# Kernel optimization log

Hardware: AMD Instinct MI355X
Metric: run time of the kernel (lower is better)

The kernel has to match this reference:

```python
import jax, jax.numpy as jnp
import numpy as np

N = 100000   # nodes
E = 1600000  # edges (avg degree 16)
D = 128      # feature dim (in_size == out_size)
L = 3        # n_layers

def setup_inputs() -> dict:
    key = jax.random.key(0)
    k0, k1, k2, k3, k4 = jax.random.split(key, 5)
    x = jax.random.normal(k0, (N, D), dtype=jnp.float32)
    src = jax.random.randint(k1, (E,), 0, N)
    dst = jax.random.randint(k2, (E,), 0, N)
    # positive edge weights (DGL EdgeWeightNorm requires nonnegative)
    edge_weight = jax.random.uniform(k3, (E,), dtype=jnp.float32) + 0.1
    W = jax.random.normal(k4, (L, D, D), dtype=jnp.float32) / np.float32(np.sqrt(D))
    b = jnp.zeros((L, D), dtype=jnp.float32)
    return {"x": x, "edge_weight": edge_weight, "W": W, "b": b, "src": src, "dst": dst}

def reference(x, edge_weight, W, b, src, dst):
    n = x.shape[0]
    # EdgeWeightNorm(norm='both'): w_ij / sqrt(deg_out_w(src_i) * deg_in_w(dst_j))
    deg_src = jax.ops.segment_sum(edge_weight, src, num_segments=n)  # weighted out-degree
    deg_dst = jax.ops.segment_sum(edge_weight, dst, num_segments=n)  # weighted in-degree
    nw = edge_weight * jax.lax.rsqrt(deg_src[src] * deg_dst[dst])    # [E]
    h = x
    for i in range(W.shape[0]):
        # GraphConv(norm='none'): transform, weighted-sum aggregate, bias, ELU
        h = h @ W[i]                                   # [N, D]
        msg = h[src] * nw[:, None]                     # [E, D] gather + scale
        h = jax.ops.segment_sum(msg, dst, num_segments=n) + b[i]
        h = jax.nn.elu(h)
    return h
```

## Files before the change

### kernel.cpp

```cpp
#include <hip/hip_runtime.h>
#include <hip/hip_bf16.h>


#define D128 128
#define PBLK 256
#define BUCKET_SHIFT 8
#define DCAP 7168

typedef __attribute__((ext_vector_type(8))) short s8v;
typedef __attribute__((ext_vector_type(16))) float f16v;

__device__ __forceinline__ float elu1(float x) {
    return x > 0.f ? x : (expf(x) - 1.f);
}

__device__ __forceinline__ unsigned short bf16_rne(float v) {
    unsigned u = __float_as_uint(v);
    return (unsigned short)((u + 0x7fffu + ((u >> 16) & 1u)) >> 16);
}


__global__ __launch_bounds__(256) void part_hist2(
    const int* __restrict__ src, const int* __restrict__ dst,
    int* __restrict__ histT2, int E, int nb, int chunk, int hlen) {
    extern __shared__ int sh[];
    for (int i = threadIdx.x; i < 2 * nb; i += 256) sh[i] = 0;
    __syncthreads();
    int b = blockIdx.x;
    int beg = b * chunk, end = min(E, beg + chunk);
    for (int e = beg + threadIdx.x; e < end; e += 256) {
        atomicAdd(&sh[dst[e] >> BUCKET_SHIFT], 1);
        atomicAdd(&sh[nb + (src[e] >> BUCKET_SHIFT)], 1);
    }
    __syncthreads();
    for (int i = threadIdx.x; i < nb; i += 256)
        histT2[i * PBLK + b] = sh[i];
    for (int i = threadIdx.x; i < nb; i += 256)
        histT2[hlen + i * PBLK + b] = sh[nb + i];
}

__global__ __launch_bounds__(256) void scan_block(
    int* __restrict__ data, int* __restrict__ blockSums, int n) {
    __shared__ int tmp[256];
    int gid = blockIdx.x * 256 + threadIdx.x;
    int v = (gid < n) ? data[gid] : 0;
    tmp[threadIdx.x] = v;
    __syncthreads();
    for (int off = 1; off < 256; off <<= 1) {
        int t = (threadIdx.x >= off) ? tmp[threadIdx.x - off] : 0;
        __syncthreads();
        tmp[threadIdx.x] += t;
        __syncthreads();
    }
    if (gid < n) data[gid] = tmp[threadIdx.x] - v;
    if (threadIdx.x == 255) blockSums[blockIdx.x] = tmp[255];
}

__global__ __launch_bounds__(1024) void scan_sums(int* __restrict__ bsums, int nb) {
    __shared__ int tmp[1024];
    int v = (threadIdx.x < nb) ? bsums[threadIdx.x] : 0;
    tmp[threadIdx.x] = v;
    __syncthreads();
    for (int off = 1; off < 1024; off <<= 1) {
        int t = (threadIdx.x >= off) ? tmp[threadIdx.x - off] : 0;
        __syncthreads();
        tmp[threadIdx.x] += t;
        __syncthreads();
    }
    if (threadIdx.x < nb) bsums[threadIdx.x] = tmp[threadIdx.x] - v;
}

__global__ __launch_bounds__(256) void part_scatter2(
    const int* __restrict__ src, const int* __restrict__ dst,
    const float* __restrict__ w, const int* __restrict__ offsT2,
    const int* __restrict__ bsums,
    int2* __restrict__ pkw, int2* __restrict__ skw,
    int E, int nb, int chunk, int hlen) {
    extern __shared__ int cur[];
    int b = blockIdx.x;
    for (int i = threadIdx.x; i < nb; i += 256)
        cur[i] = offsT2[i * PBLK + b] + bsums[i];
    for (int i = threadIdx.x; i < nb; i += 256)
        cur[nb + i] = offsT2[hlen + i * PBLK + b] + bsums[nb + i] - E;
    __syncthreads();
    int beg = b * chunk, end = min(E, beg + chunk);
    for (int e = beg + threadIdx.x; e < end; e += 256) {
        int d = dst[e];
        int s = src[e];
        int wv = __float_as_int(w[e]);
        int kd = d >> BUCKET_SHIFT;
        int pos = atomicAdd(&cur[kd], 1);
        pkw[pos] = make_int2((int)((unsigned)s | ((unsigned)(d & 255) << 24)), wv);
        int ks = s >> BUCKET_SHIFT;
        int posS = atomicAdd(&cur[nb + ks], 1);
        skw[posS] = make_int2(s & 255, wv);
    }
}

__global__ __launch_bounds__(256) void bucket_sumS(
    const int2* __restrict__ skw, const int* __restrict__ offsT2,
    const int* __restrict__ bsums,
    float* __restrict__ deg_src, int E, int nb, int N, int hlen) {
    __shared__ float wsum[256];
    int k = blockIdx.x;
    int base = offsT2[hlen + k * PBLK] + bsums[nb + k] - E;
    int end = (k + 1 < nb) ? (offsT2[hlen + (k + 1) * PBLK] + bsums[nb + k + 1] - E) : E;
    int t = threadIdx.x;
    wsum[t] = 0.f;
    __syncthreads();
    for (int i = base + t; i < end; i += 256) {
        int2 v = skw[i];
        atomicAdd(&wsum[v.x], __int_as_float(v.y));
    }
    __syncthreads();
    int node = (k << BUCKET_SHIFT) + t;
    if (node < N) deg_src[node] = wsum[t];
}

__global__ __launch_bounds__(256) void bucket_build(
    const int2* __restrict__ pkw, const int* __restrict__ offsT,
    const int* __restrict__ bsums, const float* __restrict__ deg_src,
    int* __restrict__ row_start, int2* __restrict__ edata,
    int E, int nb, int N) {
    __shared__ int cnt[256];
    __shared__ float wsum[256];
    __shared__ int loc[256];
    __shared__ int cur2[256];
    extern __shared__ int2 stage[];

    int k = blockIdx.x;
    int base = offsT[k * PBLK] + bsums[k];
    int end = (k + 1 < nb) ? (offsT[(k + 1) * PBLK] + bsums[k + 1]) : E;
    int m = end - base;
    int t = threadIdx.x;
    cnt[t] = 0;
    wsum[t] = 0.f;
    __syncthreads();
    bool staged = (m <= DCAP);
    for (int i = t; i < m; i += 256) {
        int2 kw = pkw[base + i];
        if (staged) stage[i] = kw;
        int dl = (unsigned)kw.x >> 24;
        atomicAdd(&cnt[dl], 1);
        atomicAdd(&wsum[dl], __int_as_float(kw.y));
    }
    __syncthreads();
    int v = cnt[t];
    loc[t] = v;
    __syncthreads();
    for (int off = 1; off < 256; off <<= 1) {
        int tv = (t >= off) ? loc[t - off] : 0;
        __syncthreads();
        loc[t] += tv;
        __syncthreads();
    }
    int excl = loc[t] - v;
    loc[t] = excl;
    cur2[t] = 0;
    int node = (k << BUCKET_SHIFT) + t;
    if (node < N) row_start[node] = base + excl;
    if (k == 0 && t == 0) row_start[N] = E;
    __syncthreads();
    for (int i = t; i < m; i += 256) {
        int2 kw = staged ? stage[i] : pkw[base + i];
        int dl = (unsigned)kw.x >> 24;
        int s = kw.x & 0xFFFFFF;
        int pos = base + loc[dl] + atomicAdd(&cur2[dl], 1);
        float nw = __int_as_float(kw.y) * rsqrtf(deg_src[s] * wsum[dl]);
        edata[pos] = make_int2(s, __float_as_int(nw));
    }
}


__global__ __launch_bounds__(256) void prep_w(
    const float* __restrict__ W, unsigned short* __restrict__ Wh,
    unsigned short* __restrict__ Wl, int total) {
    int i = blockIdx.x * 256 + threadIdx.x;
    if (i >= total) return;
    int l = i >> 14;
    int rem = i & 16383;
    int k = rem >> 7, nn = rem & 127;
    float v = W[i];
    unsigned short h = bf16_rne(v);
    float fh = __uint_as_float((unsigned)h << 16);
    unsigned short lo = bf16_rne(v - fh);
    size_t oi = ((((size_t)l * 16 + (k >> 3)) * 128 + nn) << 3) + (k & 7);
    Wh[oi] = h;
    Wl[oi] = lo;
}

__global__ __launch_bounds__(256) void gemm_mfma_f32(
    const float* __restrict__ A, const unsigned short* __restrict__ Wh,
    const unsigned short* __restrict__ Wl, unsigned short* __restrict__ Hb,
    int n) {
    __shared__ s8v lds_hi[16][32];
    __shared__ s8v lds_lo[16][32];
    const int t = threadIdx.x;
    const int r0 = blockIdx.x * 32;
    const int l = t & 63;
    const int wv = t >> 6;
    const int n0 = wv * 32;
    const int lr = l & 31, lh = l >> 5;

    s8v bh[8], bl[8];
#pragma unroll
    for (int k0 = 0; k0 < 8; ++k0) {
        int kc = k0 * 2 + lh;
        size_t gi = ((size_t)kc * 128 + n0 + lr) << 3;
        bh[k0] = *(const s8v*)(Wh + gi);
        bl[k0] = *(const s8v*)(Wl + gi);
    }

    {
        int row = t >> 3;
        int kc0 = t & 7;
        int r = r0 + row;
#pragma unroll
        for (int hhalf = 0; hhalf < 2; ++hhalf) {
            int kc = kc0 + 8 * hhalf;
            float4 v0 = make_float4(0.f, 0.f, 0.f, 0.f), v1 = v0;
            if (r < n) {
                const float4* ap = (const float4*)(A + (size_t)r * D128 + kc * 8);
                v0 = ap[0];
                v1 = ap[1];
            }
            s8v sh, sl;
#pragma unroll
            for (int e = 0; e < 8; ++e) {
                float v = (e < 4) ? ((const float*)&v0)[e] : ((const float*)&v1)[e - 4];
                unsigned short h = bf16_rne(v);
                float fh = __uint_as_float((unsigned)h << 16);
                sh[e] = (short)h;
                sl[e] = (short)bf16_rne(v - fh);
            }
            lds_hi[kc][row ^ (kc & 7)] = sh;
            lds_lo[kc][row ^ (kc & 7)] = sl;
        }
    }
    __syncthreads();

    f16v acc = {0.f, 0.f, 0.f, 0.f, 0.f, 0.f, 0.f, 0.f,
                0.f, 0.f, 0.f, 0.f, 0.f, 0.f, 0.f, 0.f};
#pragma unroll
    for (int k0 = 0; k0 < 8; ++k0) {
        int kc = k0 * 2 + lh;
        s8v ah = lds_hi[kc][lr ^ (kc & 7)];
        s8v al = lds_lo[kc][lr ^ (kc & 7)];
        acc = __builtin_amdgcn_mfma_f32_32x32x16_bf16(ah, bh[k0], acc, 0, 0, 0);
        acc = __builtin_amdgcn_mfma_f32_32x32x16_bf16(ah, bl[k0], acc, 0, 0, 0);
        acc = __builtin_amdgcn_mfma_f32_32x32x16_bf16(al, bh[k0], acc, 0, 0, 0);
    }

#pragma unroll
    for (int rg = 0; rg < 16; ++rg) {
        int grow = r0 + (rg & 3) + 8 * (rg >> 2) + 4 * lh;
        if (grow < n) Hb[(size_t)grow * D128 + n0 + lr] = bf16_rne(acc[rg]);
    }
}

__global__ __launch_bounds__(256) void gemm_mfma_bf16(
    const unsigned short* __restrict__ A, const unsigned short* __restrict__ Wh,
    const unsigned short* __restrict__ Wl, unsigned short* __restrict__ Hb,
    int n) {
    __shared__ s8v lds_a[16][64];
    const int t = threadIdx.x;
    const int r0 = blockIdx.x * 64;
    const int l = t & 63;
    const int wv = t >> 6;
    const int n0 = wv * 32;
    const int lr = l & 31, lh = l >> 5;

    s8v bh[8], bl[8];
#pragma unroll
    for (int k0 = 0; k0 < 8; ++k0) {
        int kc = k0 * 2 + lh;
        size_t gi = ((size_t)kc * 128 + n0 + lr) << 3;
        bh[k0] = *(const s8v*)(Wh + gi);
        bl[k0] = *(const s8v*)(Wl + gi);
    }

#pragma unroll
    for (int g4 = 0; g4 < 4; ++g4) {
        int g = t * 4 + g4;
        int row = g >> 4, kc = g & 15;
        int r = r0 + row;
        s8v v = {0, 0, 0, 0, 0, 0, 0, 0};
        if (r < n) v = *(const s8v*)(A + (size_t)r * D128 + kc * 8);
        lds_a[kc][row ^ (kc & 7)] = v;
    }
    __syncthreads();

    f16v acc0 = {0.f, 0.f, 0.f, 0.f, 0.f, 0.f, 0.f, 0.f,
                 0.f, 0.f, 0.f, 0.f, 0.f, 0.f, 0.f, 0.f};
    f16v acc1 = acc0;
#pragma unroll
    for (int k0 = 0; k0 < 8; ++k0) {
        int kc = k0 * 2 + lh;
        s8v a0 = lds_a[kc][lr ^ (kc & 7)];
        s8v a1 = lds_a[kc][(32 + lr) ^ (kc & 7)];
        acc0 = __builtin_amdgcn_mfma_f32_32x32x16_bf16(a0, bh[k0], acc0, 0, 0, 0);
        acc0 = __builtin_amdgcn_mfma_f32_32x32x16_bf16(a0, bl[k0], acc0, 0, 0, 0);
        acc1 = __builtin_amdgcn_mfma_f32_32x32x16_bf16(a1, bh[k0], acc1, 0, 0, 0);
        acc1 = __builtin_amdgcn_mfma_f32_32x32x16_bf16(a1, bl[k0], acc1, 0, 0, 0);
    }

#pragma unroll
    for (int rg = 0; rg < 16; ++rg) {
        int rr = (rg & 3) + 8 * (rg >> 2) + 4 * lh;
        int grow0 = r0 + rr;
        int grow1 = r0 + 32 + rr;
        if (grow0 < n) Hb[(size_t)grow0 * D128 + n0 + lr] = bf16_rne(acc0[rg]);
        if (grow1 < n) Hb[(size_t)grow1 * D128 + n0 + lr] = bf16_rne(acc1[rg]);
    }
}


__global__ __launch_bounds__(256) void aggregate_bf16(
    const unsigned short* __restrict__ hb, const int* __restrict__ rs,
    const int2* __restrict__ edata, const float* __restrict__ bias,
    unsigned short* __restrict__ outb, float* __restrict__ outf,
    int obf, int n) {
    int wave = threadIdx.x >> 6;
    int lane = threadIdx.x & 63;
    int node = blockIdx.x * 4 + wave;
    if (node >= n) return;
    int beg = rs[node], end = rs[node + 1];
    int half = lane >> 5, c = lane & 31;
    float4 a0 = make_float4(0.f, 0.f, 0.f, 0.f);
    float4 a1 = a0, a2 = a0, a3 = a0;
    int i = beg + half;
    for (; i + 6 < end; i += 8) {
        int2 e0 = edata[i];
        int2 e1 = edata[i + 2];
        int2 e2 = edata[i + 4];
        int2 e3 = edata[i + 6];
        uint2 p0 = ((const uint2*)(hb + (size_t)e0.x * D128))[c];
        uint2 p1 = ((const uint2*)(hb + (size_t)e1.x * D128))[c];
        uint2 p2 = ((const uint2*)(hb + (size_t)e2.x * D128))[c];
        uint2 p3 = ((const uint2*)(hb + (size_t)e3.x * D128))[c];
        float w0 = __int_as_float(e0.y), w1 = __int_as_float(e1.y);
        float w2 = __int_as_float(e2.y), w3 = __int_as_float(e3.y);
        a0.x = fmaf(__uint_as_float(p0.x << 16), w0, a0.x);
        a0.y = fmaf(__uint_as_float(p0.x & 0xffff0000u), w0, a0.y);
        a0.z = fmaf(__uint_as_float(p0.y << 16), w0, a0.z);
        a0.w = fmaf(__uint_as_float(p0.y & 0xffff0000u), w0, a0.w);
        a1.x = fmaf(__uint_as_float(p1.x << 16), w1, a1.x);
        a1.y = fmaf(__uint_as_float(p1.x & 0xffff0000u), w1, a1.y);
        a1.z = fmaf(__uint_as_float(p1.y << 16), w1, a1.z);
        a1.w = fmaf(__uint_as_float(p1.y & 0xffff0000u), w1, a1.w);
        a2.x = fmaf(__uint_as_float(p2.x << 16), w2, a2.x);
        a2.y = fmaf(__uint_as_float(p2.x & 0xffff0000u), w2, a2.y);
        a2.z = fmaf(__uint_as_float(p2.y << 16), w2, a2.z);
        a2.w = fmaf(__uint_as_float(p2.y & 0xffff0000u), w2, a2.w);
        a3.x = fmaf(__uint_as_float(p3.x << 16), w3, a3.x);
        a3.y = fmaf(__uint_as_float(p3.x & 0xffff0000u), w3, a3.y);
        a3.z = fmaf(__uint_as_float(p3.y << 16), w3, a3.z);
        a3.w = fmaf(__uint_as_float(p3.y & 0xffff0000u), w3, a3.w);
    }
    for (; i < end; i += 2) {
        int2 e0 = edata[i];
        uint2 p0 = ((const uint2*)(hb + (size_t)e0.x * D128))[c];
        float w0 = __int_as_float(e0.y);
        a0.x = fmaf(__uint_as_float(p0.x << 16), w0, a0.x);
        a0.y = fmaf(__uint_as_float(p0.x & 0xffff0000u), w0, a0.y);
        a0.z = fmaf(__uint_as_float(p0.y << 16), w0, a0.z);
        a0.w = fmaf(__uint_as_float(p0.y & 0xffff0000u), w0, a0.w);
    }
    a0.x += a1.x + a2.x + a3.x;
    a0.y += a1.y + a2.y + a3.y;
    a0.z += a1.z + a2.z + a3.z;
    a0.w += a1.w + a2.w + a3.w;
    a0.x += __shfl_xor(a0.x, 32);
    a0.y += __shfl_xor(a0.y, 32);
    a0.z += __shfl_xor(a0.z, 32);
    a0.w += __shfl_xor(a0.w, 32);
    if (half == 0) {
        float4 bb = ((const float4*)bias)[c];
        float4 o;
        o.x = elu1(a0.x + bb.x);
        o.y = elu1(a0.y + bb.y);
        o.z = elu1(a0.z + bb.z);
        o.w = elu1(a0.w + bb.w);
        if (obf) {
            uint2 p;
            p.x = (unsigned)bf16_rne(o.x) | ((unsigned)bf16_rne(o.y) << 16);
            p.y = (unsigned)bf16_rne(o.z) | ((unsigned)bf16_rne(o.w) << 16);
            ((uint2*)(outb + (size_t)node * D128))[c] = p;
        } else {
            ((float4*)(outf + (size_t)node * D128))[c] = o;
        }
    }
}

extern "C" void kernel_launch(void* const* d_in, const int* in_sizes, int n_in,
                              void* d_out, int out_size, void* d_ws, size_t ws_size,
                              hipStream_t stream) {
    const float* x   = (const float*)d_in[0];
    const float* ew  = (const float*)d_in[1];
    const float* W   = (const float*)d_in[2];
    const float* b   = (const float*)d_in[3];
    const int*   src = (const int*)d_in[4];
    const int*   dst = (const int*)d_in[5];
    float* out = (float*)d_out;

    const int N = in_sizes[0] / D128;
    const int E = in_sizes[1];
    const int L = in_sizes[2] / (D128 * D128);
    const int nb = (N + 255) >> BUCKET_SHIFT;
    const int hlen = nb * PBLK;

    char* ws = (char*)d_ws;
    size_t off = 0;
    auto take = [&](size_t bytes) {
        void* p = ws + off;
        off = (off + bytes + 255) & ~(size_t)255;
        return p;
    };
    float* deg_src = (float*)take((size_t)N * 4);
    int*   histT2  = (int*)take((size_t)2 * hlen * 4);
    int*   bsums   = (int*)take(1024 * 4);
    int*   rstart  = (int*)take((size_t)(N + 1) * 4);
    int2*  edata   = (int2*)take((size_t)E * 8);
    unsigned short* Hb = (unsigned short*)take((size_t)N * D128 * 2);
    unsigned short* Ab = (unsigned short*)take((size_t)N * D128 * 2);
    unsigned short* Whg = (unsigned short*)take((size_t)L * D128 * D128 * 2);
    unsigned short* Wlg = (unsigned short*)take((size_t)L * D128 * D128 * 2);
    int2* pkw = (int2*)Ab;
    int2* skw = ((int2*)Ab) + E;

    const int chunk = (E + PBLK - 1) / PBLK;
    const int sb2 = (2 * hlen + 255) / 256;
    const size_t part_lds = (size_t)2 * nb * 4;
    const size_t dcap_lds = (size_t)DCAP * 8;

    const int wtotal = L * D128 * D128;
    prep_w<<<(wtotal + 255) / 256, 256, 0, stream>>>(W, Whg, Wlg, wtotal);

    part_hist2<<<PBLK, 256, part_lds, stream>>>(src, dst, histT2, E, nb, chunk, hlen);
    scan_block<<<sb2, 256, 0, stream>>>(histT2, bsums, 2 * hlen);
    scan_sums<<<1, 1024, 0, stream>>>(bsums, sb2);
    part_scatter2<<<PBLK, 256, part_lds, stream>>>(src, dst, ew, histT2, bsums,
                                                   pkw, skw, E, nb, chunk, hlen);
    bucket_sumS<<<nb, 256, 0, stream>>>(skw, histT2, bsums, deg_src, E, nb, N, hlen);
    bucket_build<<<nb, 256, dcap_lds, stream>>>(pkw, histT2, bsums, deg_src,
                                                rstart, edata, E, nb, N);

    const int g32 = (N + 31) / 32;
    const int g64 = (N + 63) / 64;
    const int agg_grid = (N + 3) / 4;

    gemm_mfma_f32<<<g32, 256, 0, stream>>>(x, Whg, Wlg, Hb, N);
    aggregate_bf16<<<agg_grid, 256, 0, stream>>>(Hb, rstart, edata, b,
                                                 Ab, nullptr, 1, N);
    gemm_mfma_bf16<<<g64, 256, 0, stream>>>(Ab, Whg + D128 * D128,
                                            Wlg + D128 * D128, Hb, N);
    aggregate_bf16<<<agg_grid, 256, 0, stream>>>(Hb, rstart, edata, b + D128,
                                                 Ab, nullptr, 1, N);
    gemm_mfma_bf16<<<g64, 256, 0, stream>>>(Ab, Whg + 2 * D128 * D128,
                                            Wlg + 2 * D128 * D128, Hb, N);
    aggregate_bf16<<<agg_grid, 256, 0, stream>>>(Hb, rstart, edata, b + 2 * D128,
                                                 nullptr, out, 0, N);
}
```

Baseline: 360.8 us.

## Use 16-byte gathers in aggregation, prescaled edge offsets, persistent GEMM blocks

```diff
diff --git a/kernel.cpp b/kernel.cpp
--- a/kernel.cpp
+++ b/kernel.cpp
@@ -167,7 +167,7 @@
         int s = kw.x & 0xFFFFFF;
         int pos = base + loc[dl] + atomicAdd(&cur2[dl], 1);
         float nw = __int_as_float(kw.y) * rsqrtf(deg_src[s] * wsum[dl]);
-        edata[pos] = make_int2(s, __float_as_int(nw));
+        edata[pos] = make_int2(s << 8, __float_as_int(nw));
     }
 }
 
@@ -192,11 +192,10 @@
 __global__ __launch_bounds__(256) void gemm_mfma_f32(
     const float* __restrict__ A, const unsigned short* __restrict__ Wh,
     const unsigned short* __restrict__ Wl, unsigned short* __restrict__ Hb,
-    int n) {
+    int n, int nblk) {
     __shared__ s8v lds_hi[16][32];
     __shared__ s8v lds_lo[16][32];
     const int t = threadIdx.x;
-    const int r0 = blockIdx.x * 32;
     const int l = t & 63;
     const int wv = t >> 6;
     const int n0 = wv * 32;
@@ -211,60 +210,63 @@
         bl[k0] = *(const s8v*)(Wl + gi);
     }
 
-    {
-        int row = t >> 3;
-        int kc0 = t & 7;
-        int r = r0 + row;
-#pragma unroll
-        for (int hhalf = 0; hhalf < 2; ++hhalf) {
-            int kc = kc0 + 8 * hhalf;
-            float4 v0 = make_float4(0.f, 0.f, 0.f, 0.f), v1 = v0;
-            if (r < n) {
-                const float4* ap = (const float4*)(A + (size_t)r * D128 + kc * 8);
-                v0 = ap[0];
-                v1 = ap[1];
+    const int row = t >> 3;
+    const int kc0 = t & 7;
+    for (int rb = blockIdx.x; rb < nblk; rb += gridDim.x) {
+        const int r0 = rb * 32;
+        __syncthreads();
+        {
+            int r = r0 + row;
+#pragma unroll
+            for (int hhalf = 0; hhalf < 2; ++hhalf) {
+                int kc = kc0 + 8 * hhalf;
+                float4 v0 = make_float4(0.f, 0.f, 0.f, 0.f), v1 = v0;
+                if (r < n) {
+                    const float4* ap = (const float4*)(A + (size_t)r * D128 + kc * 8);
+                    v0 = ap[0];
+                    v1 = ap[1];
+                }
+                s8v sh, sl;
+#pragma unroll
+                for (int e = 0; e < 8; ++e) {
+                    float v = (e < 4) ? ((const float*)&v0)[e] : ((const float*)&v1)[e - 4];
+                    unsigned short h = bf16_rne(v);
+                    float fh = __uint_as_float((unsigned)h << 16);
+                    sh[e] = (short)h;
+                    sl[e] = (short)bf16_rne(v - fh);
+                }
+                lds_hi[kc][row ^ (kc & 7)] = sh;
+                lds_lo[kc][row ^ (kc & 7)] = sl;
             }
-            s8v sh, sl;
-#pragma unroll
-            for (int e = 0; e < 8; ++e) {
-                float v = (e < 4) ? ((const float*)&v0)[e] : ((const float*)&v1)[e - 4];
-                unsigned short h = bf16_rne(v);
-                float fh = __uint_as_float((unsigned)h << 16);
-                sh[e] = (short)h;
-                sl[e] = (short)bf16_rne(v - fh);
-            }
-            lds_hi[kc][row ^ (kc & 7)] = sh;
-            lds_lo[kc][row ^ (kc & 7)] = sl;
-        }
-    }
-    __syncthreads();
-
-    f16v acc = {0.f, 0.f, 0.f, 0.f, 0.f, 0.f, 0.f, 0.f,
-                0.f, 0.f, 0.f, 0.f, 0.f, 0.f, 0.f, 0.f};
-#pragma unroll
-    for (int k0 = 0; k0 < 8; ++k0) {
-        int kc = k0 * 2 + lh;
-        s8v ah = lds_hi[kc][lr ^ (kc & 7)];
-        s8v al = lds_lo[kc][lr ^ (kc & 7)];
-        acc = __builtin_amdgcn_mfma_f32_32x32x16_bf16(ah, bh[k0], acc, 0, 0, 0);
-        acc = __builtin_amdgcn_mfma_f32_32x32x16_bf16(ah, bl[k0], acc, 0, 0, 0);
-        acc = __builtin_amdgcn_mfma_f32_32x32x16_bf16(al, bh[k0], acc, 0, 0, 0);
-    }
-
-#pragma unroll
-    for (int rg = 0; rg < 16; ++rg) {
-        int grow = r0 + (rg & 3) + 8 * (rg >> 2) + 4 * lh;
-        if (grow < n) Hb[(size_t)grow * D128 + n0 + lr] = bf16_rne(acc[rg]);
+        }
+        __syncthreads();
+
+        f16v acc = {0.f, 0.f, 0.f, 0.f, 0.f, 0.f, 0.f, 0.f,
+                    0.f, 0.f, 0.f, 0.f, 0.f, 0.f, 0.f, 0.f};
+#pragma unroll
+        for (int k0 = 0; k0 < 8; ++k0) {
+            int kc = k0 * 2 + lh;
+            s8v ah = lds_hi[kc][lr ^ (kc & 7)];
+            s8v al = lds_lo[kc][lr ^ (kc & 7)];
+            acc = __builtin_amdgcn_mfma_f32_32x32x16_bf16(ah, bh[k0], acc, 0, 0, 0);
+            acc = __builtin_amdgcn_mfma_f32_32x32x16_bf16(ah, bl[k0], acc, 0, 0, 0);
+            acc = __builtin_amdgcn_mfma_f32_32x32x16_bf16(al, bh[k0], acc, 0, 0, 0);
+        }
+
+#pragma unroll
+        for (int rg = 0; rg < 16; ++rg) {
+            int grow = r0 + (rg & 3) + 8 * (rg >> 2) + 4 * lh;
+            if (grow < n) Hb[(size_t)grow * D128 + n0 + lr] = bf16_rne(acc[rg]);
+        }
     }
 }
 
 __global__ __launch_bounds__(256) void gemm_mfma_bf16(
     const unsigned short* __restrict__ A, const unsigned short* __restrict__ Wh,
     const unsigned short* __restrict__ Wl, unsigned short* __restrict__ Hb,
-    int n) {
+    int n, int nblk) {
     __shared__ s8v lds_a[16][64];
     const int t = threadIdx.x;
-    const int r0 = blockIdx.x * 64;
     const int l = t & 63;
     const int wv = t >> 6;
     const int n0 = wv * 32;
@@ -279,38 +281,42 @@
         bl[k0] = *(const s8v*)(Wl + gi);
     }
 
-#pragma unroll
-    for (int g4 = 0; g4 < 4; ++g4) {
-        int g = t * 4 + g4;
-        int row = g >> 4, kc = g & 15;
-        int r = r0 + row;
-        s8v v = {0, 0, 0, 0, 0, 0, 0, 0};
-        if (r < n) v = *(const s8v*)(A + (size_t)r * D128 + kc * 8);
-        lds_a[kc][row ^ (kc & 7)] = v;
-    }
-    __syncthreads();
-
-    f16v acc0 = {0.f, 0.f, 0.f, 0.f, 0.f, 0.f, 0.f, 0.f,
-                 0.f, 0.f, 0.f, 0.f, 0.f, 0.f, 0.f, 0.f};
-    f16v acc1 = acc0;
-#pragma unroll
-    for (int k0 = 0; k0 < 8; ++k0) {
-        int kc = k0 * 2 + lh;
-        s8v a0 = lds_a[kc][lr ^ (kc & 7)];
-        s8v a1 = lds_a[kc][(32 + lr) ^ (kc & 7)];
-        acc0 = __builtin_amdgcn_mfma_f32_32x32x16_bf16(a0, bh[k0], acc0, 0, 0, 0);
-        acc0 = __builtin_amdgcn_mfma_f32_32x32x16_bf16(a0, bl[k0], acc0, 0, 0, 0);
-        acc1 = __builtin_amdgcn_mfma_f32_32x32x16_bf16(a1, bh[k0], acc1, 0, 0, 0);
-        acc1 = __builtin_amdgcn_mfma_f32_32x32x16_bf16(a1, bl[k0], acc1, 0, 0, 0);
-    }
-
-#pragma unroll
-    for (int rg = 0; rg < 16; ++rg) {
-        int rr = (rg & 3) + 8 * (rg >> 2) + 4 * lh;
-        int grow0 = r0 + rr;
-        int grow1 = r0 + 32 + rr;
-        if (grow0 < n) Hb[(size_t)grow0 * D128 + n0 + lr] = bf16_rne(acc0[rg]);
-        if (grow1 < n) Hb[(size_t)grow1 * D128 + n0 + lr] = bf16_rne(acc1[rg]);
+    for (int rb = blockIdx.x; rb < nblk; rb += gridDim.x) {
+        const int r0 = rb * 64;
+        __syncthreads();
+#pragma unroll
+        for (int g4 = 0; g4 < 4; ++g4) {
+            int g = t * 4 + g4;
+            int row = g >> 4, kc = g & 15;
+            int r = r0 + row;
+            s8v v = {0, 0, 0, 0, 0, 0, 0, 0};
+            if (r < n) v = *(const s8v*)(A + (size_t)r * D128 + kc * 8);
+            lds_a[kc][row ^ (kc & 7)] = v;
+        }
+        __syncthreads();
+
+        f16v acc0 = {0.f, 0.f, 0.f, 0.f, 0.f, 0.f, 0.f, 0.f,
+                     0.f, 0.f, 0.f, 0.f, 0.f, 0.f, 0.f, 0.f};
+        f16v acc1 = acc0;
+#pragma unroll
+        for (int k0 = 0; k0 < 8; ++k0) {
+            int kc = k0 * 2 + lh;
+            s8v a0 = lds_a[kc][lr ^ (kc & 7)];
+            s8v a1 = lds_a[kc][(32 + lr) ^ (kc & 7)];
+            acc0 = __builtin_amdgcn_mfma_f32_32x32x16_bf16(a0, bh[k0], acc0, 0, 0, 0);
+            acc0 = __builtin_amdgcn_mfma_f32_32x32x16_bf16(a0, bl[k0], acc0, 0, 0, 0);
+            acc1 = __builtin_amdgcn_mfma_f32_32x32x16_bf16(a1, bh[k0], acc1, 0, 0, 0);
+            acc1 = __builtin_amdgcn_mfma_f32_32x32x16_bf16(a1, bl[k0], acc1, 0, 0, 0);
+        }
+
+#pragma unroll
+        for (int rg = 0; rg < 16; ++rg) {
+            int rr = (rg & 3) + 8 * (rg >> 2) + 4 * lh;
+            int grow0 = r0 + rr;
+            int grow1 = r0 + 32 + rr;
+            if (grow0 < n) Hb[(size_t)grow0 * D128 + n0 + lr] = bf16_rne(acc0[rg]);
+            if (grow1 < n) Hb[(size_t)grow1 * D128 + n0 + lr] = bf16_rne(acc1[rg]);
+        }
     }
 }
 
@@ -325,69 +331,70 @@
     int node = blockIdx.x * 4 + wave;
     if (node >= n) return;
     int beg = rs[node], end = rs[node + 1];
-    int half = lane >> 5, c = lane & 31;
-    float4 a0 = make_float4(0.f, 0.f, 0.f, 0.f);
-    float4 a1 = a0, a2 = a0, a3 = a0;
-    int i = beg + half;
-    for (; i + 6 < end; i += 8) {
-        int2 e0 = edata[i];
-        int2 e1 = edata[i + 2];
-        int2 e2 = edata[i + 4];
-        int2 e3 = edata[i + 6];
-        uint2 p0 = ((const uint2*)(hb + (size_t)e0.x * D128))[c];
-        uint2 p1 = ((const uint2*)(hb + (size_t)e1.x * D128))[c];
-        uint2 p2 = ((const uint2*)(hb + (size_t)e2.x * D128))[c];
-        uint2 p3 = ((const uint2*)(hb + (size_t)e3.x * D128))[c];
+    int eg = lane >> 4;
+    int c = lane & 15;
+    const char* base = (const char*)hb + c * 16;
+    float a0[8] = {0.f, 0.f, 0.f, 0.f, 0.f, 0.f, 0.f, 0.f};
+    float a1[8] = {0.f, 0.f, 0.f, 0.f, 0.f, 0.f, 0.f, 0.f};
+    int i = beg;
+    for (; i + 7 < end; i += 8) {
+        int2 e0 = edata[i + eg];
+        int2 e1 = edata[i + 4 + eg];
+        uint4 p0 = *(const uint4*)(base + (unsigned)e0.x);
+        uint4 p1 = *(const uint4*)(base + (unsigned)e1.x);
         float w0 = __int_as_float(e0.y), w1 = __int_as_float(e1.y);
-        float w2 = __int_as_float(e2.y), w3 = __int_as_float(e3.y);
-        a0.x = fmaf(__uint_as_float(p0.x << 16), w0, a0.x);
-        a0.y = fmaf(__uint_as_float(p0.x & 0xffff0000u), w0, a0.y);
-        a0.z = fmaf(__uint_as_float(p0.y << 16), w0, a0.z);
-        a0.w = fmaf(__uint_as_float(p0.y & 0xffff0000u), w0, a0.w);
-        a1.x = fmaf(__uint_as_float(p1.x << 16), w1, a1.x);
-        a1.y = fmaf(__uint_as_float(p1.x & 0xffff0000u), w1, a1.y);
-        a1.z = fmaf(__uint_as_float(p1.y << 16), w1, a1.z);
-        a1.w = fmaf(__uint_as_float(p1.y & 0xffff0000u), w1, a1.w);
-        a2.x = fmaf(__uint_as_float(p2.x << 16), w2, a2.x);
-        a2.y = fmaf(__uint_as_float(p2.x & 0xffff0000u), w2, a2.y);
-        a2.z = fmaf(__uint_as_float(p2.y << 16), w2, a2.z);
-        a2.w = fmaf(__uint_as_float(p2.y & 0xffff0000u), w2, a2.w);
-        a3.x = fmaf(__uint_as_float(p3.x << 16), w3, a3.x);
-        a3.y = fmaf(__uint_as_float(p3.x & 0xffff0000u), w3, a3.y);
-        a3.z = fmaf(__uint_as_float(p3.y << 16), w3, a3.z);
-        a3.w = fmaf(__uint_as_float(p3.y & 0xffff0000u), w3, a3.w);
-    }
-    for (; i < end; i += 2) {
-        int2 e0 = edata[i];
-        uint2 p0 = ((const uint2*)(hb + (size_t)e0.x * D128))[c];
+#pragma unroll
+        for (int j = 0; j < 4; ++j) {
+            unsigned q0 = ((const unsigned*)&p0)[j];
+            unsigned q1 = ((const unsigned*)&p1)[j];
+            a0[2 * j]     = fmaf(__uint_as_float(q0 << 16), w0, a0[2 * j]);
+            a0[2 * j + 1] = fmaf(__uint_as_float(q0 & 0xffff0000u), w0, a0[2 * j + 1]);
+            a1[2 * j]     = fmaf(__uint_as_float(q1 << 16), w1, a1[2 * j]);
+            a1[2 * j + 1] = fmaf(__uint_as_float(q1 & 0xffff0000u), w1, a1[2 * j + 1]);
+        }
+    }
+    for (; i < end; i += 4) {
+        int idx = i + eg;
+        int2 e0 = (idx < end) ? edata[idx] : make_int2(0, 0);
+        uint4 p0 = *(const uint4*)(base + (unsigned)e0.x);
         float w0 = __int_as_float(e0.y);
-        a0.x = fmaf(__uint_as_float(p0.x << 16), w0, a0.x);
-        a0.y = fmaf(__uint_as_float(p0.x & 0xffff0000u), w0, a0.y);
-        a0.z = fmaf(__uint_as_float(p0.y << 16), w0, a0.z);
-        a0.w = fmaf(__uint_as_float(p0.y & 0xffff0000u), w0, a0.w);
-    }
-    a0.x += a1.x + a2.x + a3.x;
-    a0.y += a1.y + a2.y + a3.y;
-    a0.z += a1.z + a2.z + a3.z;
-    a0.w += a1.w + a2.w + a3.w;
-    a0.x += __shfl_xor(a0.x, 32);
-    a0.y += __shfl_xor(a0.y, 32);
-    a0.z += __shfl_xor(a0.z, 32);
-    a0.w += __shfl_xor(a0.w, 32);
-    if (half == 0) {
-        float4 bb = ((const float4*)bias)[c];
-        float4 o;
-        o.x = elu1(a0.x + bb.x);
-        o.y = elu1(a0.y + bb.y);
-        o.z = elu1(a0.z + bb.z);
-        o.w = elu1(a0.w + bb.w);
+#pragma unroll
+        for (int j = 0; j < 4; ++j) {
+            unsigned q0 = ((const unsigned*)&p0)[j];
+            a0[2 * j]     = fmaf(__uint_as_float(q0 << 16), w0, a0[2 * j]);
+            a0[2 * j + 1] = fmaf(__uint_as_float(q0 & 0xffff0000u), w0, a0[2 * j + 1]);
+        }
+    }
+#pragma unroll
+    for (int k = 0; k < 8; ++k) {
+        a0[k] += a1[k];
+        a0[k] += __shfl_xor(a0[k], 16);
+        a0[k] += __shfl_xor(a0[k], 32);
+    }
+    if (eg == 0) {
+        float4 b0 = ((const float4*)bias)[c * 2];
+        float4 b1 = ((const float4*)bias)[c * 2 + 1];
+        float o[8];
+        o[0] = elu1(a0[0] + b0.x);
+        o[1] = elu1(a0[1] + b0.y);
+        o[2] = elu1(a0[2] + b0.z);
+        o[3] = elu1(a0[3] + b0.w);
+        o[4] = elu1(a0[4] + b1.x);
+        o[5] = elu1(a0[5] + b1.y);
+        o[6] = elu1(a0[6] + b1.z);
+        o[7] = elu1(a0[7] + b1.w);
         if (obf) {
-            uint2 p;
-            p.x = (unsigned)bf16_rne(o.x) | ((unsigned)bf16_rne(o.y) << 16);
-            p.y = (unsigned)bf16_rne(o.z) | ((unsigned)bf16_rne(o.w) << 16);
-            ((uint2*)(outb + (size_t)node * D128))[c] = p;
+            uint4 p;
+            p.x = (unsigned)bf16_rne(o[0]) | ((unsigned)bf16_rne(o[1]) << 16);
+            p.y = (unsigned)bf16_rne(o[2]) | ((unsigned)bf16_rne(o[3]) << 16);
+            p.z = (unsigned)bf16_rne(o[4]) | ((unsigned)bf16_rne(o[5]) << 16);
+            p.w = (unsigned)bf16_rne(o[6]) | ((unsigned)bf16_rne(o[7]) << 16);
+            ((uint4*)(outb + (size_t)node * D128))[c] = p;
         } else {
-            ((float4*)(outf + (size_t)node * D128))[c] = o;
+            float4 q0 = make_float4(o[0], o[1], o[2], o[3]);
+            float4 q1 = make_float4(o[4], o[5], o[6], o[7]);
+            ((float4*)(outf + (size_t)node * D128))[c * 2] = q0;
+            ((float4*)(outf + (size_t)node * D128))[c * 2 + 1] = q1;
         }
     }
 }
@@ -445,19 +452,20 @@
     bucket_build<<<nb, 256, dcap_lds, stream>>>(pkw, histT2, bsums, deg_src,
                                                 rstart, edata, E, nb, N);
 
-    const int g32 = (N + 31) / 32;
-    const int g64 = (N + 63) / 64;
+    const int t32 = (N + 31) / 32;
+    const int t64 = (N + 63) / 64;
+    const int gemm_grid = 512;
     const int agg_grid = (N + 3) / 4;
 
-    gemm_mfma_f32<<<g32, 256, 0, stream>>>(x, Whg, Wlg, Hb, N);
+    gemm_mfma_f32<<<gemm_grid, 256, 0, stream>>>(x, Whg, Wlg, Hb, N, t32);
     aggregate_bf16<<<agg_grid, 256, 0, stream>>>(Hb, rstart, edata, b,
                                                  Ab, nullptr, 1, N);
-    gemm_mfma_bf16<<<g64, 256, 0, stream>>>(Ab, Whg + D128 * D128,
-                                            Wlg + D128 * D128, Hb, N);
+    gemm_mfma_bf16<<<gemm_grid, 256, 0, stream>>>(Ab, Whg + D128 * D128,
+                                                  Wlg + D128 * D128, Hb, N, t64);
     aggregate_bf16<<<agg_grid, 256, 0, stream>>>(Hb, rstart, edata, b + D128,
                                                  Ab, nullptr, 1, N);
-    gemm_mfma_bf16<<<g64, 256, 0, stream>>>(Ab, Whg + 2 * D128 * D128,
-                                            Wlg + 2 * D128 * D128, Hb, N);
+    gemm_mfma_bf16<<<gemm_grid, 256, 0, stream>>>(Ab, Whg + 2 * D128 * D128,
+                                                  Wlg + 2 * D128 * D128, Hb, N, t64);
     aggregate_bf16<<<agg_grid, 256, 0, stream>>>(Hb, rstart, edata, b + 2 * D128,
                                                  nullptr, out, 0, N);
 }
```

Measured after the change: 350.9 us. 1.03x faster.
